# Kernel optimization log

Hardware: AMD Instinct MI355X
Metric: run time of the kernel (lower is better)

## Reference

```python
import jax, jax.numpy as jnp
import numpy as np

B, D, G, N = 256, 512, 64, 8   # batch, latent_dim, num_on_states, n_states
K = G * N                      # total codebook entries


def setup_inputs() -> dict:
    key = jax.random.key(0)
    k1, k2, k3, k4 = jax.random.split(key, 4)
    input_mu = jax.random.normal(k1, (B, D), dtype=jnp.float32)
    input_logsig = 0.5 * jax.random.normal(k2, (B, D), dtype=jnp.float32)
    # codebook init, matching the torch module: mus ~ 3*N(0,1), sigs ~ 3*exp(2*N(0,1))
    on_mus = 3.0 * jax.random.normal(k3, (K, D), dtype=jnp.float32)
    on_sigs = 3.0 * jnp.exp(2.0 * jax.random.normal(k4, (K, D), dtype=jnp.float32))
    on_states = jnp.stack([on_mus, on_sigs], axis=-1)  # [K, D, 2]
    return {"input_mu": input_mu, "input_logsig": input_logsig, "on_states": on_states}


def _w2_sq_all(input_mu, input_sig, mus, sigs):
    """Squared 2-Wasserstein dist between diag Gaussians, for all (codebook k, batch b).
    Returns [K, B] = ||mu_k - mu_b||^2 + ||sig_k - sig_b||^2, via the expanded form
    so the whole per-entry python loop collapses into two GEMMs."""
    d = (jnp.sum(mus**2, -1)[:, None] + jnp.sum(input_mu**2, -1)[None, :]
         - 2.0 * mus @ input_mu.T)
    d = d + (jnp.sum(sigs**2, -1)[:, None] + jnp.sum(input_sig**2, -1)[None, :]
             - 2.0 * sigs @ input_sig.T)
    return d


def reference(input_mu, input_logsig, on_states):
    # mode is fixed to 'softmin' (the differentiable branch of the torch module)
    Bv = input_mu.shape[0]
    input_sig = jnp.exp(input_logsig)
    mus, sigs = on_states[:, :, 0], on_states[:, :, 1]          # [K, D] each

    d_kb = _w2_sq_all(input_mu, input_sig, mus, sigs)           # [K, B]
    # faithful to torch: torch.stack(dists).view(B, -1) reshapes [K,B] -> [B,K]
    dists = d_kb.reshape(Bv, -1)                                # [B, K]

    dists_g = dists.reshape(Bv, G, N)                           # contiguous groups of n_states
    softs = jax.nn.softmax(-dists_g, axis=2)                    # F.softmin over each group
    # weighted combination of (mu, sigma) states per group
    states = jnp.einsum('bgn,gnde->bgde', softs, on_states.reshape(G, N, D, 2))  # [B,G,D,2]
    dists_bg = jnp.sum(softs * dists_g, axis=2)                 # [B, G]

    # final soft assignment: F.softmin(dists, dim=0) -> softmax over the BATCH axis (faithful)
    ps = jax.nn.softmax(-dists_bg, axis=0)                      # [B, G]
    # torch.matmul(ps[B,G], states[B,G,D]) broadcasts ps -> result [B, B, D]
    quantised_mu = jnp.einsum('bg,xgd->xbd', ps, states[..., 0])   # [B, B, D]
    quantised_sig = jnp.einsum('bg,xgd->xbd', ps, states[..., 1])  # [B, B, D]
    dist = jnp.sum(dists_bg * ps, axis=1)                       # [B]
    return ((quantised_mu, quantised_sig), dists_bg, dist)
```

## Files before the change

kernel.cpp:

```cpp
#include <hip/hip_runtime.h>
#include <cstddef>
#include <cstdint>

typedef short bf16x8 __attribute__((ext_vector_type(8)));
typedef float f32x4 __attribute__((ext_vector_type(4)));

#define Bsz 256
#define Dsz 512
#define Gsz 64
#define Ksz 512

#define WS_DFLAT 0
#define WS_SOFTS 131072
#define WS_BNORM 278528
#define WS_CNORM 278784
#define WS_PSB   279296
#define WS_ONB   287488
#define WS_ZB    549632

#define ONB_STRIDE 262144
#define ZB_STRIDE  131072

#define OUT_QMU  0
#define OUT_QSIG 33554432
#define OUT_DBG  67108864
#define OUT_DIST 67125248

__device__ __forceinline__ unsigned short f2bf(float f) {
  unsigned int u = __float_as_uint(f);
  u = (u + 0x7FFFu + ((u >> 16) & 1u)) >> 16;
  return (unsigned short)u;
}
__device__ __forceinline__ float bf2f(unsigned short h) {
  return __uint_as_float(((unsigned int)h) << 16);
}

__global__ __launch_bounds__(256) void k_prep(const float* __restrict__ mu,
                                              const float* __restrict__ ls,
                                              const float* __restrict__ on,
                                              float* __restrict__ ws) {
  int t = threadIdx.x;
  __shared__ float red[256];
  if (blockIdx.x < 512) {
    int k = blockIdx.x;
    float4 v = *(const float4*)(on + (size_t)k * 1024 + 4 * t);
    unsigned short* onb0 = (unsigned short*)(ws + WS_ONB);
    unsigned short* onb1 = onb0 + ONB_STRIDE;
    *(ushort2*)&onb0[(size_t)k * 512 + 2 * t] = make_ushort2(f2bf(v.x), f2bf(v.z));
    *(ushort2*)&onb1[(size_t)k * 512 + 2 * t] = make_ushort2(f2bf(v.y), f2bf(v.w));
    red[t] = v.x * v.x + v.y * v.y + v.z * v.z + v.w * v.w;
    __syncthreads();
    for (int off = 128; off > 0; off >>= 1) {
      if (t < off) red[t] += red[t + off];
      __syncthreads();
    }
    if (t == 0) ws[WS_CNORM + k] = red[0];
  } else {
    int b = blockIdx.x - 512;
    unsigned short* zb0 = (unsigned short*)(ws + WS_ZB);
    unsigned short* zb1 = zb0 + ZB_STRIDE;
    float part = 0.f;
    for (int d = t; d < Dsz; d += 256) {
      float m = mu[b * Dsz + d];
      float s = expf(ls[b * Dsz + d]);
      zb0[(size_t)b * 512 + d] = f2bf(m);
      zb1[(size_t)b * 512 + d] = f2bf(s);
      part += m * m + s * s;
    }
    red[t] = part;
    __syncthreads();
    for (int off = 128; off > 0; off >>= 1) {
      if (t < off) red[t] += red[t + off];
      __syncthreads();
    }
    if (t == 0) ws[WS_BNORM + b] = red[0];
  }
}

__global__ __launch_bounds__(256) void k_dkb(float* __restrict__ ws,
                                             float* __restrict__ out) {
  __shared__ float pl[4][16][33];
  int t = threadIdx.x, l = t & 63, w = t >> 6;
  int lr = l & 15, lh = l >> 4;
  if (blockIdx.x == 0) out[OUT_DIST + t] = 0.f;
  int kt = blockIdx.x >> 3, bt = blockIdx.x & 7;
  int k0 = kt * 16, b0 = bt * 32;
  const unsigned short* Ap =
      (const unsigned short*)(ws + WS_ONB) + (size_t)(w >> 1) * ONB_STRIDE + (size_t)k0 * 512;
  const unsigned short* Bp =
      (const unsigned short*)(ws + WS_ZB) + (size_t)(w >> 1) * ZB_STRIDE + (size_t)b0 * 512;
  int dbase = (w & 1) * 256;

  f32x4 acc[2];
#pragma unroll
  for (int j = 0; j < 2; ++j) { acc[j][0] = 0.f; acc[j][1] = 0.f; acc[j][2] = 0.f; acc[j][3] = 0.f; }

#pragma unroll
  for (int kk = 0; kk < 8; ++kk) {
    int dl = dbase + kk * 32 + lh * 8;
    bf16x8 a0 = *(const bf16x8*)(Ap + (size_t)lr * 512 + dl);
    bf16x8 q0 = *(const bf16x8*)(Bp + (size_t)lr * 512 + dl);
    bf16x8 q1 = *(const bf16x8*)(Bp + (size_t)(lr + 16) * 512 + dl);
    acc[0] = __builtin_amdgcn_mfma_f32_16x16x32_bf16(a0, q0, acc[0], 0, 0, 0);
    acc[1] = __builtin_amdgcn_mfma_f32_16x16x32_bf16(a0, q1, acc[1], 0, 0, 0);
  }

#pragma unroll
  for (int j = 0; j < 2; ++j)
#pragma unroll
    for (int r = 0; r < 4; ++r)
      pl[w][lh * 4 + r][j * 16 + lr] = acc[j][r];
  __syncthreads();

  int r = t >> 4, c = (t & 15) * 2;
  float s0 = pl[0][r][c] + pl[1][r][c] + pl[2][r][c] + pl[3][r][c];
  float s1 = pl[0][r][c + 1] + pl[1][r][c + 1] + pl[2][r][c + 1] + pl[3][r][c + 1];
  float cn = ws[WS_CNORM + k0 + r];
  float2 o = make_float2(cn + ws[WS_BNORM + b0 + c] - 2.f * s0,
                         cn + ws[WS_BNORM + b0 + c + 1] - 2.f * s1);
  *(float2*)&ws[WS_DFLAT + (size_t)(k0 + r) * 256 + b0 + c] = o;
}

__global__ __launch_bounds__(256) void k_sm(float* __restrict__ ws,
                                            float* __restrict__ out) {
  int g = blockIdx.x, t = threadIdx.x;
  const float* df = ws + WS_DFLAT;
  int k = 2 * t + (g >> 5);
  int col = (g & 31) << 3;
  const float* p = df + (size_t)k * 256 + col;
  float4 v0 = *(const float4*)p;
  float4 v1 = *(const float4*)(p + 4);
  float d[8] = {v0.x, v0.y, v0.z, v0.w, v1.x, v1.y, v1.z, v1.w};
  float m = d[0];
#pragma unroll
  for (int n = 1; n < 8; ++n) m = fminf(m, d[n]);
  float wv[8], s = 0.f, wd = 0.f;
#pragma unroll
  for (int n = 0; n < 8; ++n) {
    wv[n] = expf(m - d[n]);
    s += wv[n];
    wd += wv[n] * d[n];
  }
  float inv = 1.f / s;
  float* so = ws + WS_SOFTS + (size_t)t * 512 + g * 8;
  *(float4*)so = make_float4(wv[0] * inv, wv[1] * inv, wv[2] * inv, wv[3] * inv);
  *(float4*)(so + 4) = make_float4(wv[4] * inv, wv[5] * inv, wv[6] * inv, wv[7] * inv);
  float dbg = wd * inv;
  out[OUT_DBG + t * 64 + g] = dbg;

  __shared__ float red[256];
  red[t] = dbg;
  __syncthreads();
  for (int off = 128; off > 0; off >>= 1) {
    if (t < off) red[t] = fminf(red[t], red[t + off]);
    __syncthreads();
  }
  float mm = red[0];
  __syncthreads();
  float wp = expf(mm - dbg);
  red[t] = wp;
  __syncthreads();
  for (int off = 128; off > 0; off >>= 1) {
    if (t < off) red[t] += red[t + off];
    __syncthreads();
  }
  float psv = wp / red[0];
  ((unsigned short*)(ws + WS_PSB))[t * 64 + g] = f2bf(psv);
  atomicAdd(&out[OUT_DIST + t], psv * dbg);
}

__global__ __launch_bounds__(256) void k_quant(const float* __restrict__ ws,
                                               float* __restrict__ out) {
  __shared__ __align__(16) unsigned short st[2][4096];
  __shared__ float sxl[576];
  int x = blockIdx.x >> 3, dt = blockIdx.x & 7;
  int dBase = dt * 64;
  int t = threadIdx.x, l = t & 63, w = t >> 6;
  int lr = l & 15, lh = l >> 4;

  const unsigned short* psb = (const unsigned short*)(ws + WS_PSB);
  bf16x8 bn[4][2];
#pragma unroll
  for (int j = 0; j < 4; ++j)
#pragma unroll
    for (int kk = 0; kk < 2; ++kk)
      bn[j][kk] = *(const bf16x8*)&psb[(size_t)(w * 64 + j * 16 + lr) * 64 + kk * 32 + lh * 8];

  {
    int i0 = t, i1 = t + 256;
    sxl[(i0 >> 3) * 9 + (i0 & 7)] = ws[WS_SOFTS + (size_t)x * 512 + i0];
    sxl[(i1 >> 3) * 9 + (i1 & 7)] = ws[WS_SOFTS + (size_t)x * 512 + i1];
  }
  __syncthreads();

  int dq = t & 15, gq = t >> 4;
#pragma unroll 1
  for (int e = 0; e < 2; ++e) {
    const unsigned short* ob =
        (const unsigned short*)(ws + WS_ONB) + (size_t)e * ONB_STRIDE + dBase + dq * 4;
    float av[4][4];
#pragma unroll
    for (int gg = 0; gg < 4; ++gg) {
      int g = gq * 4 + gg;
      float a0 = 0.f, a1 = 0.f, a2 = 0.f, a3 = 0.f;
      const unsigned short* rp = ob + (size_t)(g * 8) * 512;
#pragma unroll
      for (int n = 0; n < 8; ++n) {
        ushort4 vv = *(const ushort4*)(rp + (size_t)n * 512);
        float swv = sxl[g * 9 + n];
        a0 += swv * bf2f(vv.x);
        a1 += swv * bf2f(vv.y);
        a2 += swv * bf2f(vv.z);
        a3 += swv * bf2f(vv.w);
      }
      av[gg][0] = a0; av[gg][1] = a1; av[gg][2] = a2; av[gg][3] = a3;
    }
#pragma unroll
    for (int dd = 0; dd < 4; ++dd) {
      int d = dq * 4 + dd;
      ushort4 o = make_ushort4(f2bf(av[0][dd]), f2bf(av[1][dd]), f2bf(av[2][dd]), f2bf(av[3][dd]));
      *(ushort4*)&st[e][(d * 64 + gq * 4) ^ ((d & 7) << 3)] = o;
    }
  }
  __syncthreads();

#pragma unroll 1
  for (int e = 0; e < 2; ++e) {
    bf16x8 am[4][2];
#pragma unroll
    for (int i = 0; i < 4; ++i)
#pragma unroll
      for (int kk = 0; kk < 2; ++kk)
        am[i][kk] = *(const bf16x8*)&st[e][((i * 16 + lr) * 64 + kk * 32 + lh * 8) ^ ((lr & 7) << 3)];

    f32x4 acc[4][4];
#pragma unroll
    for (int i = 0; i < 4; ++i)
#pragma unroll
      for (int j = 0; j < 4; ++j) {
        acc[i][j][0] = 0.f; acc[i][j][1] = 0.f; acc[i][j][2] = 0.f; acc[i][j][3] = 0.f;
      }
#pragma unroll
    for (int kk = 0; kk < 2; ++kk)
#pragma unroll
      for (int i = 0; i < 4; ++i)
#pragma unroll
        for (int j = 0; j < 4; ++j)
          acc[i][j] = __builtin_amdgcn_mfma_f32_16x16x32_bf16(am[i][kk], bn[j][kk], acc[i][j], 0, 0, 0);

    float* op = out + (e ? (size_t)OUT_QSIG : (size_t)OUT_QMU) + (size_t)x * (256 * 512);
#pragma unroll
    for (int i = 0; i < 4; ++i)
#pragma unroll
      for (int j = 0; j < 4; ++j) {
        size_t off = (size_t)(w * 64 + j * 16 + lr) * 512 + dBase + i * 16 + lh * 4;
        *(f32x4*)&op[off] = acc[i][j];
      }
  }
}

extern "C" void kernel_launch(void* const* d_in, const int* in_sizes, int n_in,
                              void* d_out, int out_size, void* d_ws, size_t ws_size,
                              hipStream_t stream) {
  (void)in_sizes; (void)n_in; (void)out_size; (void)ws_size;
  const float* mu = (const float*)d_in[0];
  const float* ls = (const float*)d_in[1];
  const float* on = (const float*)d_in[2];
  float* out = (float*)d_out;
  float* ws = (float*)d_ws;

  k_prep<<<dim3(768), dim3(256), 0, stream>>>(mu, ls, on, ws);
  k_dkb<<<dim3(256), dim3(256), 0, stream>>>(ws, out);
  k_sm<<<dim3(64), dim3(256), 0, stream>>>(ws, out);
  k_quant<<<dim3(2048), dim3(256), 0, stream>>>(ws, out);
}
```

Baseline: 87.95 us.

## Precompute per-group softmin-weighted states once, then run quant GEMM from bf16 states

Adds a k_states kernel that computes the softmin-weighted combination of each group's 8 codebook states for every batch row once and stores it as bf16 in workspace. k_quant_s then only loads these precomputed states and runs the MFMA GEMM with ps. Before this, each of the 8 d-tiles in k_quant recomputed the weighted sums. The ps buffer is also rewritten in a fragment-friendly layout so B operands load contiguously. This costs an extra launch, a 32 MB workspace round-trip, and a second bf16 rounding of the states. It falls back to the old path if the workspace is too small.

```diff
diff --git a/kernel.cpp b/kernel.cpp
--- a/kernel.cpp
+++ b/kernel.cpp
@@ -17,9 +17,11 @@
 #define WS_PSB   279296
 #define WS_ONB   287488
 #define WS_ZB    549632
+#define WS_S     680704
 
 #define ONB_STRIDE 262144
 #define ZB_STRIDE  131072
+#define WS_S_NEED  ((size_t)WS_S * 4 + 33554432u)
 
 #define OUT_QMU  0
 #define OUT_QSIG 33554432
@@ -33,6 +35,10 @@
 }
 __device__ __forceinline__ float bf2f(unsigned short h) {
   return __uint_as_float(((unsigned int)h) << 16);
+}
+__device__ __forceinline__ int psb_idx(int b, int g) {
+  return ((b >> 6) << 12) | (((b >> 4) & 3) << 10) | ((g >> 5) << 9) |
+         (((g >> 3) & 3) << 7) | ((b & 15) << 3) | (g & 7);
 }
 
 __global__ __launch_bounds__(256) void k_prep(const float* __restrict__ mu,
@@ -165,12 +171,141 @@
     __syncthreads();
   }
   float psv = wp / red[0];
-  ((unsigned short*)(ws + WS_PSB))[t * 64 + g] = f2bf(psv);
+  ((unsigned short*)(ws + WS_PSB))[psb_idx(t, g)] = f2bf(psv);
   atomicAdd(&out[OUT_DIST + t], psv * dbg);
 }
 
-__global__ __launch_bounds__(256) void k_quant(const float* __restrict__ ws,
-                                               float* __restrict__ out) {
+__global__ __launch_bounds__(256) void k_states(float* __restrict__ ws) {
+  __shared__ __align__(16) unsigned short ol[8192];
+  int g = blockIdx.x >> 2, xq = blockIdx.x & 3;
+  int t = threadIdx.x;
+  {
+    int row = t >> 4, e = row >> 3, n = row & 7;
+    int d0 = (t & 15) * 32;
+    const unsigned short* src = (const unsigned short*)(ws + WS_ONB) +
+                                (size_t)e * ONB_STRIDE + (size_t)(g * 8 + n) * 512 + d0;
+#pragma unroll
+    for (int q = 0; q < 4; ++q) {
+      bf16x8 v = *(const bf16x8*)(src + q * 8);
+#pragma unroll
+      for (int i = 0; i < 8; ++i) {
+        int ed = e * 512 + d0 + q * 8 + i;
+        ol[(ed * 8 + n) ^ (((ed >> 6) & 15) << 3)] = (unsigned short)v[i];
+      }
+    }
+  }
+  int edg = t & 15, xg = t >> 4;
+  float sf[4][8];
+#pragma unroll
+  for (int xi = 0; xi < 4; ++xi) {
+    int x = xq * 64 + xg * 4 + xi;
+    float4 s0 = *(const float4*)&ws[WS_SOFTS + (size_t)x * 512 + g * 8];
+    float4 s1 = *(const float4*)&ws[WS_SOFTS + (size_t)x * 512 + g * 8 + 4];
+    sf[xi][0] = s0.x; sf[xi][1] = s0.y; sf[xi][2] = s0.z; sf[xi][3] = s0.w;
+    sf[xi][4] = s1.x; sf[xi][5] = s1.y; sf[xi][6] = s1.z; sf[xi][7] = s1.w;
+  }
+  __syncthreads();
+
+  unsigned short* Sp = (unsigned short*)(ws + WS_S);
+#pragma unroll 1
+  for (int cb = 0; cb < 8; ++cb) {
+    bf16x8 op[4];
+#pragma unroll
+    for (int cc = 0; cc < 8; ++cc) {
+      int ed = edg * 64 + cb * 8 + cc;
+      bf16x8 v = *(const bf16x8*)&ol[(ed * 8) ^ (((ed >> 6) & 15) << 3)];
+      float vf[8];
+#pragma unroll
+      for (int n = 0; n < 8; ++n) vf[n] = bf2f((unsigned short)v[n]);
+#pragma unroll
+      for (int xi = 0; xi < 4; ++xi) {
+        float a = 0.f;
+#pragma unroll
+        for (int n = 0; n < 8; ++n) a += sf[xi][n] * vf[n];
+        op[xi][cc] = (short)f2bf(a);
+      }
+    }
+#pragma unroll
+    for (int xi = 0; xi < 4; ++xi) {
+      size_t idx = ((size_t)g * 256 + xq * 64 + xg * 4 + xi) * 1024 + edg * 64 + cb * 8;
+      *(bf16x8*)&Sp[idx] = op[xi];
+    }
+  }
+}
+
+__global__ __launch_bounds__(256) void k_quant_s(const float* __restrict__ ws,
+                                                 float* __restrict__ out) {
+  __shared__ __align__(16) unsigned short st[8192];
+  int x = blockIdx.x >> 3, dt = blockIdx.x & 7;
+  int dBase = dt * 64;
+  int t = threadIdx.x, l = t & 63, w = t >> 6;
+  int lr = l & 15, lh = l >> 4;
+
+  const unsigned short* psb = (const unsigned short*)(ws + WS_PSB);
+  bf16x8 bn[4][2];
+#pragma unroll
+  for (int j = 0; j < 4; ++j)
+#pragma unroll
+    for (int kk = 0; kk < 2; ++kk)
+      bn[j][kk] = *(const bf16x8*)&psb[w * 4096 + j * 1024 + kk * 512 + l * 8];
+
+  {
+    int gp = t >> 2, e = (t >> 1) & 1, half = t & 1;
+    const unsigned short* s0 = (const unsigned short*)(ws + WS_S) +
+                               ((size_t)(gp * 2) * 256 + x) * 1024 + e * 512 + dBase + half * 32;
+    const unsigned short* s1 = s0 + 262144;
+#pragma unroll
+    for (int q = 0; q < 4; ++q) {
+      bf16x8 v0 = *(const bf16x8*)(s0 + q * 8);
+      bf16x8 v1 = *(const bf16x8*)(s1 + q * 8);
+#pragma unroll
+      for (int i = 0; i < 8; ++i) {
+        int d = half * 32 + q * 8 + i;
+        ushort2 pr = make_ushort2((unsigned short)v0[i], (unsigned short)v1[i]);
+        *(ushort2*)&st[d * 128 + e * 64 + ((gp * 2) ^ ((d & 7) << 3))] = pr;
+      }
+    }
+  }
+  __syncthreads();
+
+#pragma unroll 1
+  for (int e = 0; e < 2; ++e) {
+    bf16x8 am[4][2];
+#pragma unroll
+    for (int i = 0; i < 4; ++i)
+#pragma unroll
+      for (int kk = 0; kk < 2; ++kk)
+        am[i][kk] = *(const bf16x8*)&st[(i * 16 + lr) * 128 + e * 64 +
+                                        ((kk * 32 + lh * 8) ^ ((lr & 7) << 3))];
+
+    f32x4 acc[4][4];
+#pragma unroll
+    for (int i = 0; i < 4; ++i)
+#pragma unroll
+      for (int j = 0; j < 4; ++j) {
+        acc[i][j][0] = 0.f; acc[i][j][1] = 0.f; acc[i][j][2] = 0.f; acc[i][j][3] = 0.f;
+      }
+#pragma unroll
+    for (int kk = 0; kk < 2; ++kk)
+#pragma unroll
+      for (int i = 0; i < 4; ++i)
+#pragma unroll
+        for (int j = 0; j < 4; ++j)
+          acc[i][j] = __builtin_amdgcn_mfma_f32_16x16x32_bf16(am[i][kk], bn[j][kk], acc[i][j], 0, 0, 0);
+
+    float* op = out + (e ? (size_t)OUT_QSIG : (size_t)OUT_QMU) + (size_t)x * (256 * 512);
+#pragma unroll
+    for (int i = 0; i < 4; ++i)
+#pragma unroll
+      for (int j = 0; j < 4; ++j) {
+        size_t off = (size_t)(w * 64 + j * 16 + lr) * 512 + dBase + i * 16 + lh * 4;
+        *(f32x4*)&op[off] = acc[i][j];
+      }
+  }
+}
+
+__global__ __launch_bounds__(256) void k_quant_f(const float* __restrict__ ws,
+                                                 float* __restrict__ out) {
   __shared__ __align__(16) unsigned short st[2][4096];
   __shared__ float sxl[576];
   int x = blockIdx.x >> 3, dt = blockIdx.x & 7;
@@ -184,12 +319,12 @@
   for (int j = 0; j < 4; ++j)
 #pragma unroll
     for (int kk = 0; kk < 2; ++kk)
-      bn[j][kk] = *(const bf16x8*)&psb[(size_t)(w * 64 + j * 16 + lr) * 64 + kk * 32 + lh * 8];
+      bn[j][kk] = *(const bf16x8*)&psb[w * 4096 + j * 1024 + kk * 512 + l * 8];
 
   {
     int i0 = t, i1 = t + 256;
     sxl[(i0 >> 3) * 9 + (i0 & 7)] = ws[WS_SOFTS + (size_t)x * 512 + i0];
-    sxl[(i1 >> 3) * 9 + (i1 & 7)] = ws[WS_SOFTS + (size_t)x * 512 + i1];
+    sxl[(i1 >> 3) * 9 + (i1 & 7)] = ws[WS_SOFTS + (size_t)x * 512 + 256 + i0];
   }
   __syncthreads();
 
@@ -262,7 +397,7 @@
 extern "C" void kernel_launch(void* const* d_in, const int* in_sizes, int n_in,
                               void* d_out, int out_size, void* d_ws, size_t ws_size,
                               hipStream_t stream) {
-  (void)in_sizes; (void)n_in; (void)out_size; (void)ws_size;
+  (void)in_sizes; (void)n_in; (void)out_size;
   const float* mu = (const float*)d_in[0];
   const float* ls = (const float*)d_in[1];
   const float* on = (const float*)d_in[2];
@@ -272,5 +407,10 @@
   k_prep<<<dim3(768), dim3(256), 0, stream>>>(mu, ls, on, ws);
   k_dkb<<<dim3(256), dim3(256), 0, stream>>>(ws, out);
   k_sm<<<dim3(64), dim3(256), 0, stream>>>(ws, out);
-  k_quant<<<dim3(2048), dim3(256), 0, stream>>>(ws, out);
-}
+  if (ws_size >= WS_S_NEED) {
+    k_states<<<dim3(256), dim3(256), 0, stream>>>(ws);
+    k_quant_s<<<dim3(2048), dim3(256), 0, stream>>>(ws, out);
+  } else {
+    k_quant_f<<<dim3(2048), dim3(256), 0, stream>>>(ws, out);
+  }
+}
```

Result: slower. 124.2 us (+41.3%).

## Fuse prep, distance GEMM and softmin into one cooperative kernel

Applied to the files above, without the earlier changes.

Merges the three front kernels (bf16 conversion and norms, distance MFMA, group softmin plus batch softmax) into a single cooperative launch separated by grid.sync, removing two kernel launch boundaries. It also stores the bf16 ps matrix in a swizzled tile order so k_quant loads each MFMA operand as one contiguous 16-byte chunk per lane. Grid syncs across 768 blocks cost something of their own, and a cooperative launch requires every block to be co-resident.

```diff
diff --git a/kernel.cpp b/kernel.cpp
--- a/kernel.cpp
+++ b/kernel.cpp
@@ -1,6 +1,9 @@
 #include <hip/hip_runtime.h>
+#include <hip/hip_cooperative_groups.h>
 #include <cstddef>
 #include <cstdint>
+
+namespace cg = cooperative_groups;
 
 typedef short bf16x8 __attribute__((ext_vector_type(8)));
 typedef float f32x4 __attribute__((ext_vector_type(4)));
@@ -34,139 +37,149 @@
 __device__ __forceinline__ float bf2f(unsigned short h) {
   return __uint_as_float(((unsigned int)h) << 16);
 }
-
-__global__ __launch_bounds__(256) void k_prep(const float* __restrict__ mu,
-                                              const float* __restrict__ ls,
-                                              const float* __restrict__ on,
-                                              float* __restrict__ ws) {
-  int t = threadIdx.x;
-  __shared__ float red[256];
-  if (blockIdx.x < 512) {
-    int k = blockIdx.x;
-    float4 v = *(const float4*)(on + (size_t)k * 1024 + 4 * t);
-    unsigned short* onb0 = (unsigned short*)(ws + WS_ONB);
-    unsigned short* onb1 = onb0 + ONB_STRIDE;
-    *(ushort2*)&onb0[(size_t)k * 512 + 2 * t] = make_ushort2(f2bf(v.x), f2bf(v.z));
-    *(ushort2*)&onb1[(size_t)k * 512 + 2 * t] = make_ushort2(f2bf(v.y), f2bf(v.w));
-    red[t] = v.x * v.x + v.y * v.y + v.z * v.z + v.w * v.w;
+__device__ __forceinline__ int psb_idx(int b, int g) {
+  return ((b >> 6) << 12) | (((b >> 4) & 3) << 10) | ((g >> 5) << 9) |
+         (((g >> 3) & 3) << 7) | ((b & 15) << 3) | (g & 7);
+}
+
+__global__ __launch_bounds__(256) void k_front(const float* __restrict__ mu,
+                                               const float* __restrict__ ls,
+                                               const float* __restrict__ on,
+                                               float* __restrict__ ws,
+                                               float* __restrict__ out) {
+  __shared__ __align__(16) char smem[4 * 16 * 33 * 4];
+  cg::grid_group grid = cg::this_grid();
+  int bid = blockIdx.x, t = threadIdx.x;
+
+  {
+    float* red = (float*)smem;
+    if (bid < 512) {
+      int k = bid;
+      float4 v = *(const float4*)(on + (size_t)k * 1024 + 4 * t);
+      unsigned short* onb0 = (unsigned short*)(ws + WS_ONB);
+      unsigned short* onb1 = onb0 + ONB_STRIDE;
+      *(ushort2*)&onb0[(size_t)k * 512 + 2 * t] = make_ushort2(f2bf(v.x), f2bf(v.z));
+      *(ushort2*)&onb1[(size_t)k * 512 + 2 * t] = make_ushort2(f2bf(v.y), f2bf(v.w));
+      red[t] = v.x * v.x + v.y * v.y + v.z * v.z + v.w * v.w;
+      __syncthreads();
+      for (int off = 128; off > 0; off >>= 1) {
+        if (t < off) red[t] += red[t + off];
+        __syncthreads();
+      }
+      if (t == 0) ws[WS_CNORM + k] = red[0];
+    } else {
+      int b = bid - 512;
+      unsigned short* zb0 = (unsigned short*)(ws + WS_ZB);
+      unsigned short* zb1 = zb0 + ZB_STRIDE;
+      float part = 0.f;
+      for (int d = t; d < Dsz; d += 256) {
+        float m = mu[b * Dsz + d];
+        float s = expf(ls[b * Dsz + d]);
+        zb0[(size_t)b * 512 + d] = f2bf(m);
+        zb1[(size_t)b * 512 + d] = f2bf(s);
+        part += m * m + s * s;
+      }
+      red[t] = part;
+      __syncthreads();
+      for (int off = 128; off > 0; off >>= 1) {
+        if (t < off) red[t] += red[t + off];
+        __syncthreads();
+      }
+      if (t == 0) ws[WS_BNORM + b] = red[0];
+    }
+  }
+  grid.sync();
+
+  if (bid < 256) {
+    float (*pl)[16][33] = (float (*)[16][33])smem;
+    int l = t & 63, w = t >> 6;
+    int lr = l & 15, lh = l >> 4;
+    if (bid == 0) out[OUT_DIST + t] = 0.f;
+    int kt = bid >> 3, bt = bid & 7;
+    int k0 = kt * 16, b0 = bt * 32;
+    const unsigned short* Ap =
+        (const unsigned short*)(ws + WS_ONB) + (size_t)(w >> 1) * ONB_STRIDE + (size_t)k0 * 512;
+    const unsigned short* Bp =
+        (const unsigned short*)(ws + WS_ZB) + (size_t)(w >> 1) * ZB_STRIDE + (size_t)b0 * 512;
+    int dbase = (w & 1) * 256;
+
+    f32x4 acc[2];
+#pragma unroll
+    for (int j = 0; j < 2; ++j) { acc[j][0] = 0.f; acc[j][1] = 0.f; acc[j][2] = 0.f; acc[j][3] = 0.f; }
+
+#pragma unroll
+    for (int kk = 0; kk < 8; ++kk) {
+      int dl = dbase + kk * 32 + lh * 8;
+      bf16x8 a0 = *(const bf16x8*)(Ap + (size_t)lr * 512 + dl);
+      bf16x8 q0 = *(const bf16x8*)(Bp + (size_t)lr * 512 + dl);
+      bf16x8 q1 = *(const bf16x8*)(Bp + (size_t)(lr + 16) * 512 + dl);
+      acc[0] = __builtin_amdgcn_mfma_f32_16x16x32_bf16(a0, q0, acc[0], 0, 0, 0);
+      acc[1] = __builtin_amdgcn_mfma_f32_16x16x32_bf16(a0, q1, acc[1], 0, 0, 0);
+    }
+
+#pragma unroll
+    for (int j = 0; j < 2; ++j)
+#pragma unroll
+      for (int r = 0; r < 4; ++r)
+        pl[w][lh * 4 + r][j * 16 + lr] = acc[j][r];
+    __syncthreads();
+
+    int r = t >> 4, c = (t & 15) * 2;
+    float s0 = pl[0][r][c] + pl[1][r][c] + pl[2][r][c] + pl[3][r][c];
+    float s1 = pl[0][r][c + 1] + pl[1][r][c + 1] + pl[2][r][c + 1] + pl[3][r][c + 1];
+    float cn = ws[WS_CNORM + k0 + r];
+    float2 o = make_float2(cn + ws[WS_BNORM + b0 + c] - 2.f * s0,
+                           cn + ws[WS_BNORM + b0 + c + 1] - 2.f * s1);
+    *(float2*)&ws[WS_DFLAT + (size_t)(k0 + r) * 256 + b0 + c] = o;
+  }
+  grid.sync();
+
+  if (bid < 64) {
+    float* red = (float*)smem;
+    int g = bid;
+    const float* df = ws + WS_DFLAT;
+    int k = 2 * t + (g >> 5);
+    int col = (g & 31) << 3;
+    const float* p = df + (size_t)k * 256 + col;
+    float4 v0 = *(const float4*)p;
+    float4 v1 = *(const float4*)(p + 4);
+    float d[8] = {v0.x, v0.y, v0.z, v0.w, v1.x, v1.y, v1.z, v1.w};
+    float m = d[0];
+#pragma unroll
+    for (int n = 1; n < 8; ++n) m = fminf(m, d[n]);
+    float wv[8], s = 0.f, wd = 0.f;
+#pragma unroll
+    for (int n = 0; n < 8; ++n) {
+      wv[n] = expf(m - d[n]);
+      s += wv[n];
+      wd += wv[n] * d[n];
+    }
+    float inv = 1.f / s;
+    float* so = ws + WS_SOFTS + (size_t)t * 512 + g * 8;
+    *(float4*)so = make_float4(wv[0] * inv, wv[1] * inv, wv[2] * inv, wv[3] * inv);
+    *(float4*)(so + 4) = make_float4(wv[4] * inv, wv[5] * inv, wv[6] * inv, wv[7] * inv);
+    float dbg = wd * inv;
+    out[OUT_DBG + t * 64 + g] = dbg;
+
+    red[t] = dbg;
+    __syncthreads();
+    for (int off = 128; off > 0; off >>= 1) {
+      if (t < off) red[t] = fminf(red[t], red[t + off]);
+      __syncthreads();
+    }
+    float mm = red[0];
+    __syncthreads();
+    float wp = expf(mm - dbg);
+    red[t] = wp;
     __syncthreads();
     for (int off = 128; off > 0; off >>= 1) {
       if (t < off) red[t] += red[t + off];
       __syncthreads();
     }
-    if (t == 0) ws[WS_CNORM + k] = red[0];
-  } else {
-    int b = blockIdx.x - 512;
-    unsigned short* zb0 = (unsigned short*)(ws + WS_ZB);
-    unsigned short* zb1 = zb0 + ZB_STRIDE;
-    float part = 0.f;
-    for (int d = t; d < Dsz; d += 256) {
-      float m = mu[b * Dsz + d];
-      float s = expf(ls[b * Dsz + d]);
-      zb0[(size_t)b * 512 + d] = f2bf(m);
-      zb1[(size_t)b * 512 + d] = f2bf(s);
-      part += m * m + s * s;
-    }
-    red[t] = part;
-    __syncthreads();
-    for (int off = 128; off > 0; off >>= 1) {
-      if (t < off) red[t] += red[t + off];
-      __syncthreads();
-    }
-    if (t == 0) ws[WS_BNORM + b] = red[0];
-  }
-}
-
-__global__ __launch_bounds__(256) void k_dkb(float* __restrict__ ws,
-                                             float* __restrict__ out) {
-  __shared__ float pl[4][16][33];
-  int t = threadIdx.x, l = t & 63, w = t >> 6;
-  int lr = l & 15, lh = l >> 4;
-  if (blockIdx.x == 0) out[OUT_DIST + t] = 0.f;
-  int kt = blockIdx.x >> 3, bt = blockIdx.x & 7;
-  int k0 = kt * 16, b0 = bt * 32;
-  const unsigned short* Ap =
-      (const unsigned short*)(ws + WS_ONB) + (size_t)(w >> 1) * ONB_STRIDE + (size_t)k0 * 512;
-  const unsigned short* Bp =
-      (const unsigned short*)(ws + WS_ZB) + (size_t)(w >> 1) * ZB_STRIDE + (size_t)b0 * 512;
-  int dbase = (w & 1) * 256;
-
-  f32x4 acc[2];
-#pragma unroll
-  for (int j = 0; j < 2; ++j) { acc[j][0] = 0.f; acc[j][1] = 0.f; acc[j][2] = 0.f; acc[j][3] = 0.f; }
-
-#pragma unroll
-  for (int kk = 0; kk < 8; ++kk) {
-    int dl = dbase + kk * 32 + lh * 8;
-    bf16x8 a0 = *(const bf16x8*)(Ap + (size_t)lr * 512 + dl);
-    bf16x8 q0 = *(const bf16x8*)(Bp + (size_t)lr * 512 + dl);
-    bf16x8 q1 = *(const bf16x8*)(Bp + (size_t)(lr + 16) * 512 + dl);
-    acc[0] = __builtin_amdgcn_mfma_f32_16x16x32_bf16(a0, q0, acc[0], 0, 0, 0);
-    acc[1] = __builtin_amdgcn_mfma_f32_16x16x32_bf16(a0, q1, acc[1], 0, 0, 0);
-  }
-
-#pragma unroll
-  for (int j = 0; j < 2; ++j)
-#pragma unroll
-    for (int r = 0; r < 4; ++r)
-      pl[w][lh * 4 + r][j * 16 + lr] = acc[j][r];
-  __syncthreads();
-
-  int r = t >> 4, c = (t & 15) * 2;
-  float s0 = pl[0][r][c] + pl[1][r][c] + pl[2][r][c] + pl[3][r][c];
-  float s1 = pl[0][r][c + 1] + pl[1][r][c + 1] + pl[2][r][c + 1] + pl[3][r][c + 1];
-  float cn = ws[WS_CNORM + k0 + r];
-  float2 o = make_float2(cn + ws[WS_BNORM + b0 + c] - 2.f * s0,
-                         cn + ws[WS_BNORM + b0 + c + 1] - 2.f * s1);
-  *(float2*)&ws[WS_DFLAT + (size_t)(k0 + r) * 256 + b0 + c] = o;
-}
-
-__global__ __launch_bounds__(256) void k_sm(float* __restrict__ ws,
-                                            float* __restrict__ out) {
-  int g = blockIdx.x, t = threadIdx.x;
-  const float* df = ws + WS_DFLAT;
-  int k = 2 * t + (g >> 5);
-  int col = (g & 31) << 3;
-  const float* p = df + (size_t)k * 256 + col;
-  float4 v0 = *(const float4*)p;
-  float4 v1 = *(const float4*)(p + 4);
-  float d[8] = {v0.x, v0.y, v0.z, v0.w, v1.x, v1.y, v1.z, v1.w};
-  float m = d[0];
-#pragma unroll
-  for (int n = 1; n < 8; ++n) m = fminf(m, d[n]);
-  float wv[8], s = 0.f, wd = 0.f;
-#pragma unroll
-  for (int n = 0; n < 8; ++n) {
-    wv[n] = expf(m - d[n]);
-    s += wv[n];
-    wd += wv[n] * d[n];
-  }
-  float inv = 1.f / s;
-  float* so = ws + WS_SOFTS + (size_t)t * 512 + g * 8;
-  *(float4*)so = make_float4(wv[0] * inv, wv[1] * inv, wv[2] * inv, wv[3] * inv);
-  *(float4*)(so + 4) = make_float4(wv[4] * inv, wv[5] * inv, wv[6] * inv, wv[7] * inv);
-  float dbg = wd * inv;
-  out[OUT_DBG + t * 64 + g] = dbg;
-
-  __shared__ float red[256];
-  red[t] = dbg;
-  __syncthreads();
-  for (int off = 128; off > 0; off >>= 1) {
-    if (t < off) red[t] = fminf(red[t], red[t + off]);
-    __syncthreads();
-  }
-  float mm = red[0];
-  __syncthreads();
-  float wp = expf(mm - dbg);
-  red[t] = wp;
-  __syncthreads();
-  for (int off = 128; off > 0; off >>= 1) {
-    if (t < off) red[t] += red[t + off];
-    __syncthreads();
-  }
-  float psv = wp / red[0];
-  ((unsigned short*)(ws + WS_PSB))[t * 64 + g] = f2bf(psv);
-  atomicAdd(&out[OUT_DIST + t], psv * dbg);
+    float psv = wp / red[0];
+    ((unsigned short*)(ws + WS_PSB))[psb_idx(t, g)] = f2bf(psv);
+    atomicAdd(&out[OUT_DIST + t], psv * dbg);
+  }
 }
 
 __global__ __launch_bounds__(256) void k_quant(const float* __restrict__ ws,
@@ -184,7 +197,7 @@
   for (int j = 0; j < 4; ++j)
 #pragma unroll
     for (int kk = 0; kk < 2; ++kk)
-      bn[j][kk] = *(const bf16x8*)&psb[(size_t)(w * 64 + j * 16 + lr) * 64 + kk * 32 + lh * 8];
+      bn[j][kk] = *(const bf16x8*)&psb[w * 4096 + j * 1024 + kk * 512 + l * 8];
 
   {
     int i0 = t, i1 = t + 256;
@@ -269,8 +282,7 @@
   float* out = (float*)d_out;
   float* ws = (float*)d_ws;
 
-  k_prep<<<dim3(768), dim3(256), 0, stream>>>(mu, ls, on, ws);
-  k_dkb<<<dim3(256), dim3(256), 0, stream>>>(ws, out);
-  k_sm<<<dim3(64), dim3(256), 0, stream>>>(ws, out);
+  void* args[] = {(void*)&mu, (void*)&ls, (void*)&on, (void*)&ws, (void*)&out};
+  hipLaunchCooperativeKernel((const void*)k_front, dim3(768), dim3(256), args, 0, stream);
   k_quant<<<dim3(2048), dim3(256), 0, stream>>>(ws, out);
 }
```

Measured after the change: 221.0 us. +151.2%, slower.
